# Performance work log

Hardware: AMD Instinct MI355X
Metric: run time of the kernel (lower is better)

## Reference

```python
import jax, jax.numpy as jnp
import numpy as np

BUFFER_SIZE = 1024
NUM_ITERS = 2
USE_MOMENTUM = True


def setup_inputs() -> dict:
    key = jax.random.key(0)
    visual_features = jax.random.normal(key, (4, 32, 256, 768), dtype=jnp.float32)
    return {"visual_features": visual_features}


def _kmeans_iteration(centers, data, weights):
    # centers: (B,K,D), data: (B,M,D), weights: (B,M)
    K = centers.shape[1]
    # squared euclidean distances (argmin identical to torch.cdist p=2 argmin)
    d2 = (
        jnp.sum(data * data, axis=-1)[:, :, None]
        - 2.0 * jnp.einsum("bmd,bkd->bmk", data, centers)
        + jnp.sum(centers * centers, axis=-1)[:, None, :]
    )  # (B,M,K)
    assignments = jnp.argmin(d2, axis=-1)  # (B,M)
    one_hot = jax.nn.one_hot(assignments, K, dtype=data.dtype)  # (B,M,K)
    weighted_oh = one_hot * weights[:, :, None]  # (B,M,K)
    weighted_data = jnp.einsum("bmk,bmd->bkd", weighted_oh, data)  # (B,K,D)
    new_counts = jnp.sum(weighted_oh, axis=1)  # (B,K)
    new_centers = weighted_data / (new_counts[:, :, None] + 1e-8)
    empty = new_counts < 1e-6
    new_centers = jnp.where(empty[:, :, None], centers, new_centers)
    return new_centers, new_counts


def reference(visual_features):
    B, T, N, D = visual_features.shape
    K = BUFFER_SIZE
    num_init = max(1, min(K // N, T))

    # init memory from first num_init frames
    init_feats = visual_features[:, :num_init].reshape(B, -1, D)
    memory = init_feats[:, :K]  # (B,K,D)
    counts = jnp.ones((B, K), dtype=visual_features.dtype)

    def update(carry, frame_tokens):
        mem, cnt = carry  # (B,K,D), (B,K)
        data = jnp.concatenate([mem, frame_tokens], axis=1)  # (B,K+N,D)
        if USE_MOMENTUM:
            new_w = jnp.ones((B, frame_tokens.shape[1]), dtype=data.dtype)
            weights = jnp.concatenate([cnt, new_w], axis=1)
        else:
            weights = jnp.ones((B, data.shape[1]), dtype=data.dtype)
        c, cc = mem, cnt
        for _ in range(NUM_ITERS):
            c, cc = _kmeans_iteration(c, data, weights)
        return (c, cc), None

    # scan over remaining frames: (T', B, N, D)
    frames = jnp.moveaxis(visual_features[:, num_init:], 1, 0)
    (memory, counts), _ = jax.lax.scan(update, (memory, counts), frames)
    return memory
```

## Files before the change

### kernel.cpp

```cpp
#include <hip/hip_runtime.h>

#define NB 4
#define NT 32
#define ND 768
#define NK 1024
#define NN 256
#define NINIT 4
#define NFRAMES 28
#define NM 1280

typedef _Float16 f16;
typedef f16 f16x8 __attribute__((ext_vector_type(8)));
typedef f16 f16x4 __attribute__((ext_vector_type(4)));
typedef float f32x4 __attribute__((ext_vector_type(4)));

#define GLOAD_LDS(g, s) __builtin_amdgcn_global_load_lds( \
    (const __attribute__((address_space(1))) void*)(g),   \
    (__attribute__((address_space(3))) void*)(s), 16, 0, 0)

__device__ __forceinline__ int swz(int r) { return ((r >> 1) & 3) << 4; }

__global__ __launch_bounds__(256) void k_init(
    const float* __restrict__ V, float* __restrict__ memF, float* __restrict__ cnt,
    f16* __restrict__ mH, f16* __restrict__ mL,
    float* __restrict__ cnP, unsigned long long* __restrict__ packed0,
    int* __restrict__ scoreIdxTok)
{
    int gid = blockIdx.x * 256 + threadIdx.x;
    if (gid < NB * 512) {
        int i = gid & 511;
        scoreIdxTok[gid] = (i < 256) ? NK + i : -1;
    }
    int row = blockIdx.x * 4 + (threadIdx.x >> 6);
    int lane = threadIdx.x & 63;
    int b = row >> 10, k = row & 1023;
    const float4* src = (const float4*)(V + ((size_t)b * NT * NN + k) * ND);
    float4* mrow = (float4*)(memF + (size_t)row * ND);
    f16x4* hrow = (f16x4*)(mH + (size_t)row * ND);
    f16x4* lrow = (f16x4*)(mL + (size_t)row * ND);
    float s2 = 0.f;
#pragma unroll
    for (int jj = 0; jj < 3; ++jj) {
        float4 x = src[lane + 64 * jj];
        mrow[lane + 64 * jj] = x;
        f16x4 h, lo;
        h[0] = (f16)x.x; lo[0] = (f16)(x.x - (float)h[0]);
        h[1] = (f16)x.y; lo[1] = (f16)(x.y - (float)h[1]);
        h[2] = (f16)x.z; lo[2] = (f16)(x.z - (float)h[2]);
        h[3] = (f16)x.w; lo[3] = (f16)(x.w - (float)h[3]);
        hrow[lane + 64 * jj] = h;
        lrow[lane + 64 * jj] = lo;
        s2 += x.x * x.x + x.y * x.y + x.z * x.z + x.w * x.w;
    }
#pragma unroll
    for (int off = 32; off; off >>= 1) s2 += __shfl_xor(s2, off);
    if (lane == 0) {
        cnP[row * 3] = s2; cnP[row * 3 + 1] = 0.f; cnP[row * 3 + 2] = 0.f;
        cnt[row] = 1.0f; packed0[(size_t)b * NM + k] = ~0ull;
    }
    if (lane == 1 && k < NN) packed0[(size_t)b * NM + NK + k] = ~0ull;
}

__global__ __launch_bounds__(256) void k_prep(
    const float* __restrict__ V, int t0, int nF,
    f16* __restrict__ tokH, f16* __restrict__ tokL, size_t tokBS)
{
    int g = blockIdx.x * 4 + (threadIdx.x >> 6);
    int lane = threadIdx.x & 63;
    int perB = nF * NN;
    if (g >= NB * perB) return;
    int b = g / perB;
    int rem = g - b * perB;
    int fi = rem / NN, n = rem - fi * NN;
    const float4* src = (const float4*)(V + (((size_t)b * NT + t0 + fi) * NN + n) * ND);
    f16x4* hrow = (f16x4*)(tokH + (size_t)b * tokBS + (size_t)(fi * NN + n) * ND);
    f16x4* lrow = (f16x4*)(tokL + (size_t)b * tokBS + (size_t)(fi * NN + n) * ND);
#pragma unroll
    for (int jj = 0; jj < 3; ++jj) {
        float4 x = src[lane + 64 * jj];
        f16x4 h, lo;
        h[0] = (f16)x.x; lo[0] = (f16)(x.x - (float)h[0]);
        h[1] = (f16)x.y; lo[1] = (f16)(x.y - (float)h[1]);
        h[2] = (f16)x.z; lo[2] = (f16)(x.z - (float)h[2]);
        h[3] = (f16)x.w; lo[3] = (f16)(x.w - (float)h[3]);
        hrow[lane + 64 * jj] = h;
        lrow[lane + 64 * jj] = lo;
    }
}

__global__ __launch_bounds__(512) void k_scoreX(
    const int* __restrict__ sidx, int mTiles,
    const f16* __restrict__ MH, const f16* __restrict__ ML,
    const f16* __restrict__ TH, const f16* __restrict__ TL, size_t tokBS,
    const f16* __restrict__ BH, const f16* __restrict__ BL,
    const int* __restrict__ hitF,
    const float* __restrict__ cnP,
    unsigned long long* __restrict__ packed)
{
    constexpr int MT = 64;
    constexpr int FM = 2;
    constexpr int QROWS = 32;
    constexpr int ASL = 4;
    constexpr int SLOTS = 16;
    constexpr int SPW = 4;
    constexpr int RSZ = SLOTS * 1024;

    __shared__ float4 ldsbuf[SLOTS * 128];
    char* lds = (char*)ldsbuf;

    int bid = blockIdx.x;
    int cpx = (int)gridDim.x >> 3;
    int sz = (bid & 7) * cpx + (bid >> 3);
    int pb = mTiles * 16;
    int b = sz / pb;
    int rem = sz - b * pb;
    int mt = rem >> 4, kt = rem & 15;
    const int* sb = sidx + b * 512;
    if (sb[mt * MT] < 0) return;
    int tid = threadIdx.x;
    int w = tid >> 6, l = tid & 63;
    int h = w >> 2, q = w & 3;
    int wm = q >> 1, wk = q & 1;
    const int REG = h * RSZ;

    const char* sp[SPW];
#pragma unroll
    for (int i = 0; i < SPW; ++i) {
        int slot = q * SPW + i;
        const f16* base; int r;
        if (slot < ASL) {
            r = slot * 16 + (l >> 2);
            int rid = sb[mt * MT + r]; if (rid < 0) rid = 0;
            base = (rid < NK) ? MH + ((size_t)b * NK + rid) * ND
                              : TH + (size_t)b * tokBS + (size_t)(rid - NK) * ND;
        } else if (slot < 2 * ASL) {
            r = (slot - ASL) * 16 + (l >> 2);
            int rid = sb[mt * MT + r]; if (rid < 0) rid = 0;
            base = (rid < NK) ? ML + ((size_t)b * NK + rid) * ND
                              : TL + (size_t)b * tokBS + (size_t)(rid - NK) * ND;
        } else if (slot < 2 * ASL + 4) {
            r = (slot - 2 * ASL) * 16 + (l >> 2);
            int kc = kt * 64 + r;
            const f16* bb = BH;
            if (hitF && !hitF[b * NK + kc]) bb = MH;
            base = bb + ((size_t)b * NK + kc) * ND;
        } else {
            r = (slot - 2 * ASL - 4) * 16 + (l >> 2);
            int kc = kt * 64 + r;
            const f16* bb = BL;
            if (hitF && !hitF[b * NK + kc]) bb = ML;
            base = bb + ((size_t)b * NK + kc) * ND;
        }
        int colB = ((l & 3) * 16) ^ swz(r);
        sp[i] = (const char*)base + h * 768 + colB;
    }

    int aoffH[FM], aoffL[FM], boffH[2], boffL[2];
#pragma unroll
    for (int mi = 0; mi < FM; ++mi) {
        int r = wm * QROWS + mi * 16 + (l & 15);
        int off = r * 64 + (((l >> 4) * 16) ^ swz(r));
        aoffH[mi] = REG + off;
        aoffL[mi] = REG + ASL * 1024 + off;
    }
#pragma unroll
    for (int nj = 0; nj < 2; ++nj) {
        int rB = wk * 32 + nj * 16 + (l & 15);
        int off = rB * 64 + (((l >> 4) * 16) ^ swz(rB));
        boffH[nj] = REG + 2 * ASL * 1024 + off;
        boffL[nj] = REG + 2 * ASL * 1024 + 4096 + off;
    }

    f32x4 acc[FM][2] = {};

    for (int c = 0; c < 12; ++c) {
#pragma unroll
        for (int i = 0; i < SPW; ++i) {
            GLOAD_LDS(sp[i], lds + REG + (q * SPW + i) * 1024);
            sp[i] += 64;
        }
        __syncthreads();
        f16x8 ah[FM], al[FM], bh[2], bl[2];
#pragma unroll
        for (int mi = 0; mi < FM; ++mi) {
            ah[mi] = *(const f16x8*)(lds + aoffH[mi]);
            al[mi] = *(const f16x8*)(lds + aoffL[mi]);
        }
#pragma unroll
        for (int nj = 0; nj < 2; ++nj) {
            bh[nj] = *(const f16x8*)(lds + boffH[nj]);
            bl[nj] = *(const f16x8*)(lds + boffL[nj]);
        }
#pragma unroll
        for (int mi = 0; mi < FM; ++mi)
#pragma unroll
            for (int nj = 0; nj < 2; ++nj) {
                acc[mi][nj] = __builtin_amdgcn_mfma_f32_16x16x32_f16(ah[mi], bh[nj], acc[mi][nj], 0, 0, 0);
                acc[mi][nj] = __builtin_amdgcn_mfma_f32_16x16x32_f16(ah[mi], bl[nj], acc[mi][nj], 0, 0, 0);
                acc[mi][nj] = __builtin_amdgcn_mfma_f32_16x16x32_f16(al[mi], bh[nj], acc[mi][nj], 0, 0, 0);
            }
        __syncthreads();
    }

    int coff = q * (QROWS * 128) + l * 16;
    if (h == 1) {
#pragma unroll
        for (int mi = 0; mi < FM; ++mi)
#pragma unroll
            for (int nj = 0; nj < 2; ++nj)
                *(f32x4*)(lds + coff + (mi * 2 + nj) * 1024) = acc[mi][nj];
    }
    __syncthreads();
    if (h != 0) return;
#pragma unroll
    for (int mi = 0; mi < FM; ++mi)
#pragma unroll
        for (int nj = 0; nj < 2; ++nj)
            acc[mi][nj] += *(const f32x4*)(lds + coff + (mi * 2 + nj) * 1024);

    int colb = kt * 64 + wk * 32 + (l & 15);
    float cn[2];
#pragma unroll
    for (int nj = 0; nj < 2; ++nj) {
        int kc = b * NK + colb + nj * 16;
        cn[nj] = cnP[kc * 3] + cnP[kc * 3 + 1] + cnP[kc * 3 + 2];
    }
    size_t pbase = (size_t)b * NM;
#pragma unroll
    for (int mi = 0; mi < FM; ++mi) {
#pragma unroll
        for (int rg = 0; rg < 4; ++rg) {
            float bv = 1e30f; int bi = 0;
#pragma unroll
            for (int nj = 0; nj < 2; ++nj) {
                float s = cn[nj] - 2.0f * acc[mi][nj][rg];
                int ki = colb + nj * 16;
                if (s < bv) { bv = s; bi = ki; }
            }
#pragma unroll
            for (int off = 1; off < 16; off <<= 1) {
                float ov = __shfl_xor(bv, off);
                int   oi = __shfl_xor(bi, off);
                if (ov < bv || (ov == bv && oi < bi)) { bv = ov; bi = oi; }
            }
            if ((l & 15) == 0) {
                int Rt = mt * MT + wm * QROWS + mi * 16 + (l >> 4) * 4 + rg;
                int rid = sb[Rt];
                if (rid >= 0) {
                    unsigned u = __float_as_uint(bv);
                    unsigned key = (u >> 31) ? ~u : (u | 0x80000000u);
                    atomicMin(&packed[pbase + rid],
                              ((unsigned long long)key << 32) | (unsigned)bi);
                }
            }
        }
    }
}

__global__ __launch_bounds__(1024) void k_lists(
    const unsigned long long* __restrict__ packed, int selfSeed,
    unsigned long long* __restrict__ packedOther,
    int2* __restrict__ cb, int* __restrict__ lstIdx, int* __restrict__ ctrOf,
    int* __restrict__ totalPos, int* __restrict__ scoreIdx2,
    int* __restrict__ hitF)
{
    __shared__ int cntL[NK];
    __shared__ int wsum[16];
    __shared__ int hwsum[16];
    __shared__ int cursor[NK];
    __shared__ int aSh[NM];
    __shared__ int totSh, hitSh;
    int b = blockIdx.x, tid = threadIdx.x;
    cntL[tid] = 0;
    __syncthreads();
    if (selfSeed) {
        if (tid < NN) {
            int a = (int)(unsigned)(packed[(size_t)b * NM + NK + tid] & 0xffffffffull);
            aSh[tid] = a;
            atomicAdd(&cntL[a], 1);
        }
    } else {
        for (int m = tid; m < NM; m += 1024) {
            int a = (int)(unsigned)(packed[(size_t)b * NM + m] & 0xffffffffull);
            aSh[m] = a;
            atomicAdd(&cntL[a], 1);
        }
    }
    for (int m = tid; m < NM; m += 1024)
        packedOther[(size_t)b * NM + m] = ~0ull;
    __syncthreads();
    int v0 = cntL[tid];
    int v = selfSeed ? (v0 ? v0 + 1 : 0) : v0;
    int hit = (selfSeed && v0 > 0) ? 1 : 0;
    int lane = tid & 63, wv = tid >> 6;
    int x = v, hx = hit;
#pragma unroll
    for (int off = 1; off < 64; off <<= 1) {
        int y = __shfl_up(x, off);
        int hy = __shfl_up(hx, off);
        if (lane >= off) { x += y; hx += hy; }
    }
    if (lane == 63) { wsum[wv] = x; hwsum[wv] = hx; }
    __syncthreads();
    if (tid < 16) {
        int s = wsum[tid];
        int e = s;
#pragma unroll
        for (int off = 1; off < 16; off <<= 1) {
            int y = __shfl_up(e, off, 16);
            if (tid >= off) e += y;
        }
        wsum[tid] = e - s;
    } else if (tid < 32) {
        int s = hwsum[tid - 16];
        int e = s;
#pragma unroll
        for (int off = 1; off < 16; off <<= 1) {
            int y = __shfl_up(e, off, 16);
            if ((tid - 16) >= off) e += y;
        }
        hwsum[tid - 16] = e - s;
    }
    __syncthreads();
    int base = x + wsum[wv] - v;
    int hb = hx + hwsum[wv] - hit;
    cursor[tid] = base + ((selfSeed && v0) ? 1 : 0);
    cb[b * NK + tid] = make_int2(v, base);
    if (selfSeed && v0) {
        lstIdx[(size_t)b * NM + base] = tid;
        ctrOf[(size_t)b * NM + base] = tid;
    }
    if (selfSeed) {
        hitF[b * NK + tid] = hit;
        packedOther[(size_t)b * NM + tid] = hit ? ~0ull : (unsigned long long)(unsigned)tid;
        if (tid < NN) packedOther[(size_t)b * NM + NK + tid] = ~0ull;
        if (hit) scoreIdx2[b * 512 + 256 + hb] = tid;
        if (tid < 256) scoreIdx2[b * 512 + tid] = NK + tid;
        if (tid == 1023) hitSh = hb + hit;
    }
    if (tid == 1023) totSh = base + v;
    __syncthreads();
    if (selfSeed) {
        if (tid < NN) {
            int a = aSh[tid];
            int pos = atomicAdd(&cursor[a], 1);
            lstIdx[(size_t)b * NM + pos] = NK + tid;
            ctrOf[(size_t)b * NM + pos] = a;
        }
        int H = hitSh;
        if (tid >= H && tid < 256) scoreIdx2[b * 512 + 256 + tid] = -1;
        if (tid == 0) {
            int total = totSh;
            int padEnd = (total + 7) & ~7;
            for (int p2 = total; p2 < padEnd; ++p2) {
                lstIdx[(size_t)b * NM + p2] = 0;
                ctrOf[(size_t)b * NM + p2] = -1;
            }
            totalPos[b] = total;
        }
    } else {
        for (int m = tid; m < NM; m += 1024) {
            int a = aSh[m];
            int pos = atomicAdd(&cursor[a], 1);
            lstIdx[(size_t)b * NM + pos] = m;
            ctrOf[(size_t)b * NM + pos] = a;
        }
        if (tid == 0) totalPos[b] = NM;
    }
}

__global__ __launch_bounds__(256) void k_part(
    const float* __restrict__ memF, const float* __restrict__ V, int t,
    const float* __restrict__ cntF,
    const int* __restrict__ lstIdx, const int* __restrict__ ctrOf,
    const int* __restrict__ totalPos,
    float* __restrict__ part, float* __restrict__ partW)
{
    int g = blockIdx.x * 4 + (threadIdx.x >> 6);
    int l = threadIdx.x & 63;
    int b = g / 480;
    int rem = g - b * 480;
    int seg = rem / 3, c = rem - seg * 3;
    int pos0 = seg * 8;
    if (pos0 >= totalPos[b]) return;
    const int* li = lstIdx + (size_t)b * NM;
    const int* co = ctrOf + (size_t)b * NM;
    int ctr[8]; float wg[8]; float4 xv[8];
#pragma unroll
    for (int i = 0; i < 8; ++i) {
        int p = pos0 + i;
        int cc = co[p];
        int mm = li[p];
        bool pad = cc < 0;
        ctr[i] = pad ? -2 : cc;
        wg[i] = pad ? 0.f : ((mm < NK) ? cntF[b * NK + mm] : 1.0f);
        int mload = pad ? 0 : mm;
        const float4* dr = (mload < NK)
            ? (const float4*)(memF + ((size_t)b * NK + mload) * ND)
            : (const float4*)(V + (((size_t)b * NT + t) * NN + (mload - NK)) * (size_t)ND);
        xv[i] = dr[c * 64 + l];
    }
    float4 acc; float sw; int cur = ctr[0];
    acc.x = wg[0] * xv[0].x; acc.y = wg[0] * xv[0].y;
    acc.z = wg[0] * xv[0].z; acc.w = wg[0] * xv[0].w;
    sw = wg[0];
#pragma unroll
    for (int i = 1; i < 8; ++i) {
        if (ctr[i] != cur) {
            int e = pos0 + i - 1;
            ((float4*)(part + ((size_t)b * NM + e) * ND))[c * 64 + l] = acc;
            if (c == 0 && l == 0) partW[b * NM + e] = sw;
            cur = ctr[i];
            acc.x = wg[i] * xv[i].x; acc.y = wg[i] * xv[i].y;
            acc.z = wg[i] * xv[i].z; acc.w = wg[i] * xv[i].w;
            sw = wg[i];
        } else {
            acc.x += wg[i] * xv[i].x; acc.y += wg[i] * xv[i].y;
            acc.z += wg[i] * xv[i].z; acc.w += wg[i] * xv[i].w;
            sw += wg[i];
        }
    }
    int e = pos0 + 7;
    ((float4*)(part + ((size_t)b * NM + e) * ND))[c * 64 + l] = acc;
    if (c == 0 && l == 0) partW[b * NM + e] = sw;
}

__global__ __launch_bounds__(256) void k_upd(
    const f16* __restrict__ cenHin, const f16* __restrict__ cenLin,
    const int2* __restrict__ cb,
    const float* __restrict__ part, const float* __restrict__ partW,
    const unsigned long long* __restrict__ packedIn, int iter1Mode,
    float* __restrict__ Cout, float* __restrict__ cntOut,
    f16* __restrict__ outH, f16* __restrict__ outL,
    float* __restrict__ cnP)
{
    int g = blockIdx.x * 4 + (threadIdx.x >> 6);
    int lane = threadIdx.x & 63;
    int row = g / 3, c = g - row * 3;
    int b = row >> 10, k = row & 1023;
    int2 cnb = cb[row];
    int n = cnb.x, base = cnb.y;
    if (iter1Mode && n == 0) return;
    if (!iter1Mode && n == 1 &&
        (packedIn[(size_t)b * NM + k] >> 32) == 0)
        return;
    float4 vv;
    float sumw = 0.f;
    if (n == 0) {
        f16x4 hh = ((const f16x4*)(cenHin + (size_t)row * ND))[c * 64 + lane];
        f16x4 ll = ((const f16x4*)(cenLin + (size_t)row * ND))[c * 64 + lane];
        vv.x = (float)hh[0] + (float)ll[0];
        vv.y = (float)hh[1] + (float)ll[1];
        vv.z = (float)hh[2] + (float)ll[2];
        vv.w = (float)hh[3] + (float)ll[3];
        sumw = 0.f;
    } else {
        float4 acc = {0.f, 0.f, 0.f, 0.f};
        int last = base + n - 1;
        int s1 = last >> 3;
        for (int s = base >> 3; s <= s1; ++s) {
            int e = (8 * s + 7 < last) ? (8 * s + 7) : last;
            float4 x = ((const float4*)(part + ((size_t)b * NM + e) * ND))[c * 64 + lane];
            acc.x += x.x; acc.y += x.y; acc.z += x.z; acc.w += x.w;
            sumw += partW[b * NM + e];
        }
        float inv = 1.0f / (sumw + 1e-8f);
        vv.x = acc.x * inv; vv.y = acc.y * inv; vv.z = acc.z * inv; vv.w = acc.w * inv;
    }
    if (!iter1Mode)
        ((float4*)(Cout + (size_t)row * ND))[c * 64 + lane] = vv;
    f16x4 h, lo;
    h[0] = (f16)vv.x; lo[0] = (f16)(vv.x - (float)h[0]);
    h[1] = (f16)vv.y; lo[1] = (f16)(vv.y - (float)h[1]);
    h[2] = (f16)vv.z; lo[2] = (f16)(vv.z - (float)h[2]);
    h[3] = (f16)vv.w; lo[3] = (f16)(vv.w - (float)h[3]);
    ((f16x4*)(outH + (size_t)row * ND))[c * 64 + lane] = h;
    ((f16x4*)(outL + (size_t)row * ND))[c * 64 + lane] = lo;
    float s2 = vv.x * vv.x + vv.y * vv.y + vv.z * vv.z + vv.w * vv.w;
#pragma unroll
    for (int off = 32; off; off >>= 1) s2 += __shfl_xor(s2, off);
    if (lane == 0) cnP[row * 3 + c] = s2;
    if (lane == 0 && c == 0) cntOut[row] = sumw;
}

__global__ __launch_bounds__(256) void k_copy(const float* __restrict__ memF,
                                              float* __restrict__ out) {
    size_t i = (size_t)blockIdx.x * 256 + threadIdx.x;
    ((float4*)out)[i] = ((const float4*)memF)[i];
}

extern "C" void kernel_launch(void* const* d_in, const int* in_sizes, int n_in,
                              void* d_out, int out_size, void* d_ws, size_t ws_size,
                              hipStream_t stream) {
    const float* V = (const float*)d_in[0];
    float* out = (float*)d_out;
    char* p = (char*)d_ws;
    auto take = [&](size_t bytes) { char* r = p; p += (bytes + 255) & ~(size_t)255; return r; };

    const size_t fixedBytes = 60ull * 1024 * 1024;
    const size_t fullTokBytes = 2ull * NB * NFRAMES * NN * ND * 2;
    const bool full = ws_size >= fixedBytes + fullTokBytes;
    const size_t tokBS = full ? (size_t)NFRAMES * NN * ND : (size_t)NN * ND;

    float* memF = (float*)take((size_t)NB * NK * ND * 4);
    float* cnt  = (float*)take(NB * NK * 4);
    float* cntS = (float*)take(NB * NK * 4);
    float* cnP  = (float*)take(NB * NK * 3 * 4);
    unsigned long long* packed0 = (unsigned long long*)take(NB * NM * 8);
    unsigned long long* packed1 = (unsigned long long*)take(NB * NM * 8);
    int2* cbBuf  = (int2*)take(NB * NK * 8);
    int*  lstIdx = (int*)take(NB * NM * 4);
    int*  ctrOf  = (int*)take(NB * NM * 4);
    int*  totalPos = (int*)take(NB * 4);
    int*  scoreIdxTok = (int*)take(NB * 512 * 4);
    int*  scoreIdx2   = (int*)take(NB * 512 * 4);
    int*  hitF   = (int*)take(NB * NK * 4);
    float* partW = (float*)take(NB * NM * 4);
    float* partB = (float*)take((size_t)NB * NM * ND * 4);
    f16* memH = (f16*)take((size_t)NB * NK * ND * 2);
    f16* memL = (f16*)take((size_t)NB * NK * ND * 2);
    f16* cenH = (f16*)take((size_t)NB * NK * ND * 2);
    f16* cenL = (f16*)take((size_t)NB * NK * ND * 2);
    f16* tokH = (f16*)take((size_t)NB * tokBS * 2);
    f16* tokL = (f16*)take((size_t)NB * tokBS * 2);

    k_init<<<1024, 256, 0, stream>>>(V, memF, cnt, memH, memL, cnP, packed0, scoreIdxTok);
    if (full)
        k_prep<<<NB * NFRAMES * NN / 4, 256, 0, stream>>>(V, NINIT, NFRAMES, tokH, tokL, tokBS);

    for (int f = 0; f < NFRAMES; ++f) {
        int t = NINIT + f;
        const f16* tH = full ? tokH + (size_t)f * NN * ND : tokH;
        const f16* tL = full ? tokL + (size_t)f * NN * ND : tokL;

        if (!full)
            k_prep<<<NB * NN / 4, 256, 0, stream>>>(V, t, 1, tokH, tokL, tokBS);

        k_scoreX<<<256, 512, 0, stream>>>(scoreIdxTok, 4, memH, memL, tH, tL, tokBS,
                                          memH, memL, nullptr, cnP, packed0);
        k_lists<<<NB, 1024, 0, stream>>>(packed0, 1, packed1, cbBuf, lstIdx, ctrOf,
                                         totalPos, scoreIdx2, hitF);
        k_part<<<480, 256, 0, stream>>>(memF, V, t, cnt, lstIdx, ctrOf, totalPos, partB, partW);
        k_upd<<<3072, 256, 0, stream>>>(cenH, cenL, cbBuf, partB, partW,
                                        packed1, 1, memF, cntS, cenH, cenL, cnP);

        k_scoreX<<<512, 512, 0, stream>>>(scoreIdx2, 8, memH, memL, tH, tL, tokBS,
                                          cenH, cenL, hitF, cnP, packed1);
        k_lists<<<NB, 1024, 0, stream>>>(packed1, 0, packed0, cbBuf, lstIdx, ctrOf,
                                         totalPos, scoreIdx2, hitF);
        k_part<<<480, 256, 0, stream>>>(memF, V, t, cnt, lstIdx, ctrOf, totalPos, partB, partW);
        k_upd<<<3072, 256, 0, stream>>>(cenH, cenL, cbBuf, partB, partW,
                                        packed1, 0, memF, cnt, memH, memL, cnP);
    }

    k_copy<<<3072, 256, 0, stream>>>(memF, out);
}
```

Baseline: 2.519 ms.

## Double-buffer LDS staging in k_scoreX to overlap global loads with MFMA

Doubles the LDS buffer in the scoring kernel and prefetches the next K-chunk into the alternate buffer while the current one is consumed by MFMAs. Explicit vmcnt waits and raw s_barrier with sched_barrier replace the per-iteration __syncthreads, so load latency can hide behind compute. The cost is twice the LDS per block (64KB), which can lower occupancy, and it relies on correct manual waitcnt ordering.

```diff
diff --git a/kernel.cpp b/kernel.cpp
--- a/kernel.cpp
+++ b/kernel.cpp
@@ -105,7 +105,7 @@
     constexpr int SPW = 4;
     constexpr int RSZ = SLOTS * 1024;
 
-    __shared__ float4 ldsbuf[SLOTS * 128];
+    __shared__ float4 ldsbuf[2 * SLOTS * 128];
     char* lds = (char*)ldsbuf;
 
     int bid = blockIdx.x;
@@ -173,23 +173,34 @@
 
     f32x4 acc[FM][2] = {};
 
+#define STAGEX(bufbase)                                                   \
+    _Pragma("unroll")                                                     \
+    for (int i = 0; i < SPW; ++i) {                                       \
+        GLOAD_LDS(sp[i], lds + (bufbase) + REG + (q * SPW + i) * 1024);   \
+        sp[i] += 64;                                                      \
+    }
+
+    STAGEX(0);
     for (int c = 0; c < 12; ++c) {
-#pragma unroll
-        for (int i = 0; i < SPW; ++i) {
-            GLOAD_LDS(sp[i], lds + REG + (q * SPW + i) * 1024);
-            sp[i] += 64;
-        }
-        __syncthreads();
+        int cur = (c & 1) << 15;
+        if (c < 11) {
+            STAGEX(cur ^ 32768);
+            asm volatile("s_waitcnt vmcnt(4)" ::: "memory");
+        } else {
+            asm volatile("s_waitcnt vmcnt(0)" ::: "memory");
+        }
+        __builtin_amdgcn_s_barrier();
+        __builtin_amdgcn_sched_barrier(0);
         f16x8 ah[FM], al[FM], bh[2], bl[2];
 #pragma unroll
         for (int mi = 0; mi < FM; ++mi) {
-            ah[mi] = *(const f16x8*)(lds + aoffH[mi]);
-            al[mi] = *(const f16x8*)(lds + aoffL[mi]);
+            ah[mi] = *(const f16x8*)(lds + cur + aoffH[mi]);
+            al[mi] = *(const f16x8*)(lds + cur + aoffL[mi]);
         }
 #pragma unroll
         for (int nj = 0; nj < 2; ++nj) {
-            bh[nj] = *(const f16x8*)(lds + boffH[nj]);
-            bl[nj] = *(const f16x8*)(lds + boffL[nj]);
+            bh[nj] = *(const f16x8*)(lds + cur + boffH[nj]);
+            bl[nj] = *(const f16x8*)(lds + cur + boffL[nj]);
         }
 #pragma unroll
         for (int mi = 0; mi < FM; ++mi)
@@ -199,8 +210,10 @@
                 acc[mi][nj] = __builtin_amdgcn_mfma_f32_16x16x32_f16(ah[mi], bl[nj], acc[mi][nj], 0, 0, 0);
                 acc[mi][nj] = __builtin_amdgcn_mfma_f32_16x16x32_f16(al[mi], bh[nj], acc[mi][nj], 0, 0, 0);
             }
-        __syncthreads();
-    }
+        __builtin_amdgcn_sched_barrier(0);
+        __builtin_amdgcn_s_barrier();
+    }
+    __syncthreads();
 
     int coff = q * (QROWS * 128) + l * 16;
     if (h == 1) {
```

After: 2.371 ms. 5.9% less time.
